# Kernel tuning notes

Measured on AMD Instinct MI355X. Metric: run time of the kernel, lower is better.

## Reference

```python
import jax, jax.numpy as jnp
import numpy as np

N_NODES = 100000
N_EDGES = 1600000
VOCAB = 100000
HIDDEN = 64
OUT = 1
N_REL = 2


def _fast_rgcn_conv(h, src, dst, et, W, root, b, num_nodes, num_rel):
    # Per-relation linear transform of all nodes first (cheap: N*H*O per relation),
    # then gather the transformed source feature for each edge by its relation.
    h_rel = jnp.einsum('nh,rho->rno', h, W)            # (R, N, O)
    msg = h_rel[et, src]                                # (E, O) gather
    # FastRGCNConv 'mean' aggregation: normalize by edge count per (dst, relation)
    one_hot = jax.nn.one_hot(et, num_rel, dtype=h.dtype)            # (E, R)
    counts = jax.ops.segment_sum(one_hot, dst, num_segments=num_nodes)  # (N, R)
    norm = 1.0 / jnp.maximum(counts[dst, et], 1.0)                  # (E,)
    aggr = jax.ops.segment_sum(msg * norm[:, None], dst, num_segments=num_nodes)  # (N, O)
    return aggr + h @ root + b


def setup_inputs() -> dict:
    key = jax.random.key(0)
    k = jax.random.split(key, 8)
    x = jnp.arange(N_NODES, dtype=jnp.int64 if jax.config.read('jax_enable_x64') else jnp.int32)
    edge_index = jax.random.randint(k[0], (2, N_EDGES), 0, N_NODES)
    node_type = jax.random.randint(k[1], (N_NODES,), 0, 2)
    s_h = 1.0 / np.sqrt(HIDDEN)
    emb = jax.random.normal(k[2], (VOCAB, HIDDEN), jnp.float32)
    W1 = jax.random.normal(k[3], (N_REL, HIDDEN, HIDDEN), jnp.float32) * s_h
    root1 = jax.random.normal(k[4], (HIDDEN, HIDDEN), jnp.float32) * s_h
    b1 = jnp.zeros((HIDDEN,), jnp.float32)
    W2 = jax.random.normal(k[5], (N_REL, HIDDEN, OUT), jnp.float32) * s_h
    root2 = jax.random.normal(k[6], (HIDDEN, OUT), jnp.float32) * s_h
    b2 = jnp.zeros((OUT,), jnp.float32)
    return {"x": x, "edge_index": edge_index, "node_type": node_type,
            "emb": emb, "W1": W1, "root1": root1, "b1": b1,
            "W2": W2, "root2": root2, "b2": b2}


def reference(x, edge_index, node_type, emb, W1, root1, b1, W2, root2, b2):
    src, dst = edge_index[0], edge_index[1]
    # edge_type = 1 if same node type else 0
    et = (node_type[src] == node_type[dst]).astype(jnp.int32)
    h = emb[x]                                          # embedding lookup (N, H)
    h = _fast_rgcn_conv(h, src, dst, et, W1, root1, b1, N_NODES, N_REL)
    h = jax.nn.relu(h)
    out = _fast_rgcn_conv(h, src, dst, et, W2, root2, b2, N_NODES, N_REL)
    return out  # (N, 1)
```

## Files before the change

### kernel.cpp

```cpp
#include <hip/hip_runtime.h>

#define N_NODES 100000
#define N_EDGES 1600000
#define HIDDEN 64
#define NBKT 782
#define BKT_SHIFT 7
#define NT 391
#define TILE 4096

typedef __attribute__((ext_vector_type(8))) short short8v;
typedef __attribute__((ext_vector_type(4))) float f32x4;

__device__ __forceinline__ unsigned short f2bf(float f) {
    union { float f; unsigned u; } v; v.f = f;
    return (unsigned short)((v.u + 0x7FFFu + ((v.u >> 16) & 1u)) >> 16);
}
__device__ __forceinline__ float bf2f(unsigned short h) {
    union { unsigned u; float f; } v; v.u = ((unsigned)h) << 16;
    return v.f;
}


__global__ __launch_bounds__(256) void k_embf(const int* __restrict__ x, const float* __restrict__ emb,
                                              unsigned short* __restrict__ embbf) {
    int gid = blockIdx.x * 256 + threadIdx.x;
    int n = gid >> 4, q = gid & 15;
    if (n >= N_NODES) return;
    int row = x[n];
    float4 v = *(const float4*)&emb[(long long)row * HIDDEN + q * 4];
    ushort4 p;
    p.x = f2bf(v.x); p.y = f2bf(v.y); p.z = f2bf(v.z); p.w = f2bf(v.w);
    *(ushort4*)&embbf[n * HIDDEN + q * 4] = p;
}

__global__ __launch_bounds__(512) void k_hist(const int* __restrict__ ei,
                                              const int* __restrict__ ntype,
                                              unsigned* __restrict__ ps,
                                              int* __restrict__ tilecnt) {
    __shared__ int hist[NBKT];
    int tile = blockIdx.x, tid = threadIdx.x;
    for (int i = tid; i < NBKT; i += 512) hist[i] = 0;
    __syncthreads();
    int e0 = tile * TILE;
    int e1 = e0 + TILE; if (e1 > N_EDGES) e1 = N_EDGES;
    for (int e = e0 + tid; e < e1; e += 512) {
        int s = ei[e], d = ei[N_EDGES + e];
        int t = (ntype[s] == ntype[d]) ? 1 : 0;
        ps[e] = ((unsigned)s << 1) | (unsigned)t;
        atomicAdd(&hist[d >> BKT_SHIFT], 1);
    }
    __syncthreads();
    for (int i = tid; i < NBKT; i += 512) tilecnt[tile * NBKT + i] = hist[i];
}

__global__ __launch_bounds__(512) void k_scanA(int* __restrict__ tilecnt, int* __restrict__ btot) {
    __shared__ int sc[512];
    int b = blockIdx.x, tid = threadIdx.x;
    int v = (tid < NT) ? tilecnt[tid * NBKT + b] : 0;
    sc[tid] = v;
    __syncthreads();
    for (int off = 1; off < 512; off <<= 1) {
        int a = sc[tid];
        int p = (tid >= off) ? sc[tid - off] : 0;
        __syncthreads();
        sc[tid] = a + p;
        __syncthreads();
    }
    if (tid < NT) tilecnt[tid * NBKT + b] = sc[tid] - v;
    if (tid == 511) btot[b] = sc[511];
}

__global__ __launch_bounds__(1024) void k_scanB(const int* __restrict__ btot, int* __restrict__ bbase) {
    __shared__ int sc[1024];
    int tid = threadIdx.x;
    int v = (tid < NBKT) ? btot[tid] : 0;
    sc[tid] = v;
    __syncthreads();
    for (int off = 1; off < 1024; off <<= 1) {
        int a = sc[tid];
        int p = (tid >= off) ? sc[tid - off] : 0;
        __syncthreads();
        sc[tid] = a + p;
        __syncthreads();
    }
    if (tid < NBKT) bbase[tid] = sc[tid] - v;
}

__global__ __launch_bounds__(512) void k_place(const int* __restrict__ ei,
                                               const unsigned* __restrict__ ps,
                                               const int* __restrict__ tilecnt,
                                               const int* __restrict__ bbase,
                                               unsigned* __restrict__ tmp) {
    __shared__ int cur[NBKT];
    int tile = blockIdx.x, tid = threadIdx.x;
    for (int i = tid; i < NBKT; i += 512) cur[i] = bbase[i] + tilecnt[tile * NBKT + i];
    __syncthreads();
    int e0 = tile * TILE;
    int e1 = e0 + TILE; if (e1 > N_EDGES) e1 = N_EDGES;
    for (int e = e0 + tid; e < e1; e += 512) {
        int d = ei[N_EDGES + e];
        unsigned entry = ((unsigned)(d & 127) << 18) | ps[e];
        int pos = atomicAdd(&cur[d >> BKT_SHIFT], 1);
        tmp[pos] = entry;
    }
}

__global__ __launch_bounds__(256) void k_sort(const unsigned* __restrict__ tmp,
                                              const int* __restrict__ bbase,
                                              const int* __restrict__ btot,
                                              int* __restrict__ cnt, int* __restrict__ row_ptr,
                                              int* __restrict__ csr) {
    __shared__ int hist[256];
    __shared__ int psum[256];
    int b = blockIdx.x, tid = threadIdx.x;
    hist[tid] = 0;
    __syncthreads();
    int base = bbase[b], m = btot[b];

    for (int i = tid; i < m; i += 256) {
        unsigned pe = tmp[base + i];
        atomicAdd(&hist[(int)((pe >> 17) & 0xFE) | (int)(pe & 1)], 1);
    }
    __syncthreads();

    int h = hist[tid];
    psum[tid] = h;
    __syncthreads();
    for (int off = 1; off < 256; off <<= 1) {
        int a = psum[tid];
        int p = (tid >= off) ? psum[tid - off] : 0;
        __syncthreads();
        psum[tid] = a + p;
        __syncthreads();
    }
    int excl = psum[tid] - h;

    int node = b * 128 + (tid >> 1);
    if (node < N_NODES) {
        cnt[node * 2 + (tid & 1)] = h;
        if ((tid & 1) == 0) row_ptr[node] = base + excl;
    }
    __syncthreads();
    hist[tid] = excl;
    __syncthreads();

    for (int i = tid; i < m; i += 256) {
        unsigned pe = tmp[base + i];
        int bin = (int)((pe >> 17) & 0xFE) | (int)(pe & 1);
        int pos = base + atomicAdd(&hist[bin], 1);
        csr[pos] = (int)((pe >> 1) & 0x1FFFF);
    }
}

__global__ void k_gather1(const int* __restrict__ csr, const int* __restrict__ row_ptr,
                          const int* __restrict__ cnt, const unsigned short* __restrict__ embbf,
                          unsigned short* __restrict__ aggbf) {
    int gid = blockIdx.x * blockDim.x + threadIdx.x;
    int n = gid >> 6;
    int lane = gid & 63;
    if (n >= N_NODES) return;
    int q = lane >> 4;
    int ch = (lane & 15) * 4;
    int beg = row_ptr[n];
    int c0 = cnt[2 * n], c1 = cnt[2 * n + 1];
    int tot = c0 + c1;
    float a00 = 0.f, a01 = 0.f, a02 = 0.f, a03 = 0.f;
    float a10 = 0.f, a11 = 0.f, a12 = 0.f, a13 = 0.f;
    int jj = 0;
    for (; jj + 16 <= tot; jj += 16) {
        int j0 = jj + q, j1 = jj + 4 + q, j2 = jj + 8 + q, j3 = jj + 12 + q;
        int s0 = csr[beg + j0], s1 = csr[beg + j1], s2 = csr[beg + j2], s3 = csr[beg + j3];
        ushort4 v0 = *(const ushort4*)&embbf[s0 * HIDDEN + ch];
        ushort4 v1 = *(const ushort4*)&embbf[s1 * HIDDEN + ch];
        ushort4 v2 = *(const ushort4*)&embbf[s2 * HIDDEN + ch];
        ushort4 v3 = *(const ushort4*)&embbf[s3 * HIDDEN + ch];
        if (j0 < c0) { a00 += bf2f(v0.x); a01 += bf2f(v0.y); a02 += bf2f(v0.z); a03 += bf2f(v0.w); }
        else         { a10 += bf2f(v0.x); a11 += bf2f(v0.y); a12 += bf2f(v0.z); a13 += bf2f(v0.w); }
        if (j1 < c0) { a00 += bf2f(v1.x); a01 += bf2f(v1.y); a02 += bf2f(v1.z); a03 += bf2f(v1.w); }
        else         { a10 += bf2f(v1.x); a11 += bf2f(v1.y); a12 += bf2f(v1.z); a13 += bf2f(v1.w); }
        if (j2 < c0) { a00 += bf2f(v2.x); a01 += bf2f(v2.y); a02 += bf2f(v2.z); a03 += bf2f(v2.w); }
        else         { a10 += bf2f(v2.x); a11 += bf2f(v2.y); a12 += bf2f(v2.z); a13 += bf2f(v2.w); }
        if (j3 < c0) { a00 += bf2f(v3.x); a01 += bf2f(v3.y); a02 += bf2f(v3.z); a03 += bf2f(v3.w); }
        else         { a10 += bf2f(v3.x); a11 += bf2f(v3.y); a12 += bf2f(v3.z); a13 += bf2f(v3.w); }
    }
    for (int j = jj + q; j < tot; j += 4) {
        int s = csr[beg + j];
        ushort4 v = *(const ushort4*)&embbf[s * HIDDEN + ch];
        if (j < c0) { a00 += bf2f(v.x); a01 += bf2f(v.y); a02 += bf2f(v.z); a03 += bf2f(v.w); }
        else        { a10 += bf2f(v.x); a11 += bf2f(v.y); a12 += bf2f(v.z); a13 += bf2f(v.w); }
    }
    a00 += __shfl_xor(a00, 16); a00 += __shfl_xor(a00, 32);
    a01 += __shfl_xor(a01, 16); a01 += __shfl_xor(a01, 32);
    a02 += __shfl_xor(a02, 16); a02 += __shfl_xor(a02, 32);
    a03 += __shfl_xor(a03, 16); a03 += __shfl_xor(a03, 32);
    a10 += __shfl_xor(a10, 16); a10 += __shfl_xor(a10, 32);
    a11 += __shfl_xor(a11, 16); a11 += __shfl_xor(a11, 32);
    a12 += __shfl_xor(a12, 16); a12 += __shfl_xor(a12, 32);
    a13 += __shfl_xor(a13, 16); a13 += __shfl_xor(a13, 32);
    if (q == 0) {
        float n0 = 1.0f / (float)(c0 > 1 ? c0 : 1);
        float n1 = 1.0f / (float)(c1 > 1 ? c1 : 1);
        ushort4 w0, w1;
        w0.x = f2bf(a00 * n0); w0.y = f2bf(a01 * n0); w0.z = f2bf(a02 * n0); w0.w = f2bf(a03 * n0);
        w1.x = f2bf(a10 * n1); w1.y = f2bf(a11 * n1); w1.z = f2bf(a12 * n1); w1.w = f2bf(a13 * n1);
        *(ushort4*)&aggbf[n * 128 + ch] = w0;
        *(ushort4*)&aggbf[n * 128 + 64 + ch] = w1;
    }
}

#define KPAD 200
__global__ __launch_bounds__(256) void k_l1mfma(const unsigned short* __restrict__ embbf,
                                                const unsigned short* __restrict__ aggbf,
                                                const float* __restrict__ W1, const float* __restrict__ root1,
                                                const float* __restrict__ b1,
                                                const float* __restrict__ W2, const float* __restrict__ root2,
                                                const float* __restrict__ b2,
                                                float* __restrict__ s, float* __restrict__ out) {
    __shared__ unsigned short Bw[64][KPAD];
    int tid = threadIdx.x;
    int w = tid >> 6, lane = tid & 63;
    int nodeBase = blockIdx.x * 64;

    for (int it = 0; it < 12; ++it) {
        int f = it * 256 + tid;
        int k = f >> 4, o4 = (f & 15) * 4;
        float4 wv = (k < 128) ? *(const float4*)&W1[k * 64 + o4]
                              : *(const float4*)&root1[(k - 128) * 64 + o4];
        Bw[o4 + 0][k] = f2bf(wv.x);
        Bw[o4 + 1][k] = f2bf(wv.y);
        Bw[o4 + 2][k] = f2bf(wv.z);
        Bw[o4 + 3][k] = f2bf(wv.w);
    }
    __syncthreads();

    int r = lane & 15, g = lane >> 4;
    int node = nodeBase + w * 16 + r;
    int cn = node < N_NODES ? node : 0;
    const unsigned short* arow = &aggbf[cn * 128];
    const unsigned short* erow = &embbf[cn * HIDDEN];
    f32x4 acc0 = {0.f, 0.f, 0.f, 0.f}, acc1 = acc0, acc2 = acc0, acc3 = acc0;
#pragma unroll
    for (int ks = 0; ks < 6; ++ks) {
        int koff = ks * 32 + g * 8;
        short8v av = (ks < 4) ? *(const short8v*)&arow[koff]
                              : *(const short8v*)&erow[koff - 128];
        short8v bv0 = *(const short8v*)&Bw[r][koff];
        short8v bv1 = *(const short8v*)&Bw[16 + r][koff];
        short8v bv2 = *(const short8v*)&Bw[32 + r][koff];
        short8v bv3 = *(const short8v*)&Bw[48 + r][koff];
        acc0 = __builtin_amdgcn_mfma_f32_16x16x32_bf16(av, bv0, acc0, 0, 0, 0);
        acc1 = __builtin_amdgcn_mfma_f32_16x16x32_bf16(av, bv1, acc1, 0, 0, 0);
        acc2 = __builtin_amdgcn_mfma_f32_16x16x32_bf16(av, bv2, acc2, 0, 0, 0);
        acc3 = __builtin_amdgcn_mfma_f32_16x16x32_bf16(av, bv3, acc3, 0, 0, 0);
    }

    float b10 = b1[r], b11 = b1[16 + r], b12 = b1[32 + r], b13 = b1[48 + r];
    float w2a0 = W2[r], w2a1 = W2[16 + r], w2a2 = W2[32 + r], w2a3 = W2[48 + r];
    float w2b0 = W2[64 + r], w2b1 = W2[80 + r], w2b2 = W2[96 + r], w2b3 = W2[112 + r];
    float rr0 = root2[r], rr1 = root2[16 + r], rr2 = root2[32 + r], rr3 = root2[48 + r];
    float b2v = b2[0];
#pragma unroll
    for (int reg = 0; reg < 4; ++reg) {
        float h0 = acc0[reg] + b10; h0 = h0 > 0.f ? h0 : 0.f;
        float h1 = acc1[reg] + b11; h1 = h1 > 0.f ? h1 : 0.f;
        float h2 = acc2[reg] + b12; h2 = h2 > 0.f ? h2 : 0.f;
        float h3 = acc3[reg] + b13; h3 = h3 > 0.f ? h3 : 0.f;
        float p0 = h0 * w2a0 + h1 * w2a1 + h2 * w2a2 + h3 * w2a3;
        float p1 = h0 * w2b0 + h1 * w2b1 + h2 * w2b2 + h3 * w2b3;
        float p2 = h0 * rr0  + h1 * rr1  + h2 * rr2  + h3 * rr3;
#pragma unroll
        for (int mk = 8; mk >= 1; mk >>= 1) {
            p0 += __shfl_xor(p0, mk);
            p1 += __shfl_xor(p1, mk);
            p2 += __shfl_xor(p2, mk);
        }
        if (r == 0) {
            int nd = nodeBase + w * 16 + g * 4 + reg;
            if (nd < N_NODES) {
                s[nd] = p0;
                s[N_NODES + nd] = p1;
                out[nd] = p2 + b2v;
            }
        }
    }
}

__global__ void k_gather2(const int* __restrict__ csr, const int* __restrict__ row_ptr,
                          const int* __restrict__ cnt, const float* __restrict__ sarr,
                          float* __restrict__ out) {
    int gid = blockIdx.x * blockDim.x + threadIdx.x;
    int n = gid >> 4;
    int l = gid & 15;
    if (n >= N_NODES) return;
    int beg = row_ptr[n];
    int c0 = cnt[2 * n], c1 = cnt[2 * n + 1];
    int tot = c0 + c1;
    float n0 = 1.0f / (float)(c0 > 1 ? c0 : 1);
    float n1 = 1.0f / (float)(c1 > 1 ? c1 : 1);
    float acc = 0.f;
    for (int j = l; j < tot; j += 16) {
        int src = csr[beg + j];
        acc += (j < c0) ? sarr[src] * n0 : sarr[N_NODES + src] * n1;
    }
    acc += __shfl_xor(acc, 1);
    acc += __shfl_xor(acc, 2);
    acc += __shfl_xor(acc, 4);
    acc += __shfl_xor(acc, 8);
    if (l == 0) out[n] += acc;
}

extern "C" void kernel_launch(void* const* d_in, const int* in_sizes, int n_in,
                              void* d_out, int out_size, void* d_ws, size_t ws_size,
                              hipStream_t stream) {
    const int* x      = (const int*)d_in[0];
    const int* ei     = (const int*)d_in[1];
    const int* ntype  = (const int*)d_in[2];
    const float* emb  = (const float*)d_in[3];
    const float* W1   = (const float*)d_in[4];
    const float* root1= (const float*)d_in[5];
    const float* b1   = (const float*)d_in[6];
    const float* W2   = (const float*)d_in[7];
    const float* root2= (const float*)d_in[8];
    const float* b2   = (const float*)d_in[9];
    float* out = (float*)d_out;

    char* ws = (char*)d_ws;
    size_t off = 0;
    auto alloc = [&](size_t bytes) -> void* {
        void* p = ws + off;
        off = (off + bytes + 255) & ~(size_t)255;
        return p;
    };
    unsigned* ps           = (unsigned*)alloc((size_t)N_EDGES * sizeof(unsigned));
    int* tilecnt           = (int*)alloc((size_t)NT * NBKT * sizeof(int));
    int* btot              = (int*)alloc((size_t)NBKT * sizeof(int));
    int* bbase             = (int*)alloc((size_t)NBKT * sizeof(int));
    unsigned* tmp          = (unsigned*)alloc((size_t)N_EDGES * sizeof(unsigned));
    int* cnt               = (int*)alloc((size_t)N_NODES * 2 * sizeof(int));
    int* row_ptr           = (int*)alloc((size_t)N_NODES * sizeof(int));
    int* csr               = (int*)alloc((size_t)N_EDGES * sizeof(int));
    unsigned short* embbf  = (unsigned short*)alloc((size_t)N_NODES * HIDDEN * sizeof(unsigned short));
    unsigned short* aggbf  = (unsigned short*)alloc((size_t)N_NODES * 128 * sizeof(unsigned short));
    float* s               = (float*)alloc((size_t)N_NODES * 2 * sizeof(float));

    k_embf <<<(N_NODES * 16 + 255) / 256, 256, 0, stream>>>(x, emb, embbf);
    k_hist <<<NT, 512, 0, stream>>>(ei, ntype, ps, tilecnt);
    k_scanA<<<NBKT, 512, 0, stream>>>(tilecnt, btot);
    k_scanB<<<1, 1024, 0, stream>>>(btot, bbase);
    k_place<<<NT, 512, 0, stream>>>(ei, ps, tilecnt, bbase, tmp);
    k_sort <<<NBKT, 256, 0, stream>>>(tmp, bbase, btot, cnt, row_ptr, csr);
    k_gather1<<<(N_NODES * 64) / 256, 256, 0, stream>>>(csr, row_ptr, cnt, embbf, aggbf);
    k_l1mfma<<<(N_NODES + 63) / 64, 256, 0, stream>>>(embbf, aggbf, W1, root1, b1,
                                                      W2, root2, b2, s, out);
    k_gather2<<<(N_NODES * 16 + 255) / 256, 256, 0, stream>>>(csr, row_ptr, cnt, s, out);
}
```

Before: 149.7 us.

## Fuse layer-1 neighbor gather into MFMA GEMM kernel via shared-memory staging

Merges the per-node mean-aggregation gather into the layer-1 MFMA kernel. Each wavefront gathers its 16 nodes sequentially and writes the bf16 aggregates into an LDS tile, which then feeds the MFMA A operand directly. This removes the global aggbf round trip (write plus reread) and one kernel launch. The cost is less parallelism in the gather: one wave now walks 16 nodes serially instead of one node per wave. LDS use per block also rises, which may reduce occupancy and latency hiding for the random-access gather.

```diff
diff --git a/kernel.cpp b/kernel.cpp
--- a/kernel.cpp
+++ b/kernel.cpp
@@ -152,71 +152,18 @@
     }
 }
 
-__global__ void k_gather1(const int* __restrict__ csr, const int* __restrict__ row_ptr,
-                          const int* __restrict__ cnt, const unsigned short* __restrict__ embbf,
-                          unsigned short* __restrict__ aggbf) {
-    int gid = blockIdx.x * blockDim.x + threadIdx.x;
-    int n = gid >> 6;
-    int lane = gid & 63;
-    if (n >= N_NODES) return;
-    int q = lane >> 4;
-    int ch = (lane & 15) * 4;
-    int beg = row_ptr[n];
-    int c0 = cnt[2 * n], c1 = cnt[2 * n + 1];
-    int tot = c0 + c1;
-    float a00 = 0.f, a01 = 0.f, a02 = 0.f, a03 = 0.f;
-    float a10 = 0.f, a11 = 0.f, a12 = 0.f, a13 = 0.f;
-    int jj = 0;
-    for (; jj + 16 <= tot; jj += 16) {
-        int j0 = jj + q, j1 = jj + 4 + q, j2 = jj + 8 + q, j3 = jj + 12 + q;
-        int s0 = csr[beg + j0], s1 = csr[beg + j1], s2 = csr[beg + j2], s3 = csr[beg + j3];
-        ushort4 v0 = *(const ushort4*)&embbf[s0 * HIDDEN + ch];
-        ushort4 v1 = *(const ushort4*)&embbf[s1 * HIDDEN + ch];
-        ushort4 v2 = *(const ushort4*)&embbf[s2 * HIDDEN + ch];
-        ushort4 v3 = *(const ushort4*)&embbf[s3 * HIDDEN + ch];
-        if (j0 < c0) { a00 += bf2f(v0.x); a01 += bf2f(v0.y); a02 += bf2f(v0.z); a03 += bf2f(v0.w); }
-        else         { a10 += bf2f(v0.x); a11 += bf2f(v0.y); a12 += bf2f(v0.z); a13 += bf2f(v0.w); }
-        if (j1 < c0) { a00 += bf2f(v1.x); a01 += bf2f(v1.y); a02 += bf2f(v1.z); a03 += bf2f(v1.w); }
-        else         { a10 += bf2f(v1.x); a11 += bf2f(v1.y); a12 += bf2f(v1.z); a13 += bf2f(v1.w); }
-        if (j2 < c0) { a00 += bf2f(v2.x); a01 += bf2f(v2.y); a02 += bf2f(v2.z); a03 += bf2f(v2.w); }
-        else         { a10 += bf2f(v2.x); a11 += bf2f(v2.y); a12 += bf2f(v2.z); a13 += bf2f(v2.w); }
-        if (j3 < c0) { a00 += bf2f(v3.x); a01 += bf2f(v3.y); a02 += bf2f(v3.z); a03 += bf2f(v3.w); }
-        else         { a10 += bf2f(v3.x); a11 += bf2f(v3.y); a12 += bf2f(v3.z); a13 += bf2f(v3.w); }
-    }
-    for (int j = jj + q; j < tot; j += 4) {
-        int s = csr[beg + j];
-        ushort4 v = *(const ushort4*)&embbf[s * HIDDEN + ch];
-        if (j < c0) { a00 += bf2f(v.x); a01 += bf2f(v.y); a02 += bf2f(v.z); a03 += bf2f(v.w); }
-        else        { a10 += bf2f(v.x); a11 += bf2f(v.y); a12 += bf2f(v.z); a13 += bf2f(v.w); }
-    }
-    a00 += __shfl_xor(a00, 16); a00 += __shfl_xor(a00, 32);
-    a01 += __shfl_xor(a01, 16); a01 += __shfl_xor(a01, 32);
-    a02 += __shfl_xor(a02, 16); a02 += __shfl_xor(a02, 32);
-    a03 += __shfl_xor(a03, 16); a03 += __shfl_xor(a03, 32);
-    a10 += __shfl_xor(a10, 16); a10 += __shfl_xor(a10, 32);
-    a11 += __shfl_xor(a11, 16); a11 += __shfl_xor(a11, 32);
-    a12 += __shfl_xor(a12, 16); a12 += __shfl_xor(a12, 32);
-    a13 += __shfl_xor(a13, 16); a13 += __shfl_xor(a13, 32);
-    if (q == 0) {
-        float n0 = 1.0f / (float)(c0 > 1 ? c0 : 1);
-        float n1 = 1.0f / (float)(c1 > 1 ? c1 : 1);
-        ushort4 w0, w1;
-        w0.x = f2bf(a00 * n0); w0.y = f2bf(a01 * n0); w0.z = f2bf(a02 * n0); w0.w = f2bf(a03 * n0);
-        w1.x = f2bf(a10 * n1); w1.y = f2bf(a11 * n1); w1.z = f2bf(a12 * n1); w1.w = f2bf(a13 * n1);
-        *(ushort4*)&aggbf[n * 128 + ch] = w0;
-        *(ushort4*)&aggbf[n * 128 + 64 + ch] = w1;
-    }
-}
-
-#define KPAD 200
-__global__ __launch_bounds__(256) void k_l1mfma(const unsigned short* __restrict__ embbf,
-                                                const unsigned short* __restrict__ aggbf,
-                                                const float* __restrict__ W1, const float* __restrict__ root1,
-                                                const float* __restrict__ b1,
-                                                const float* __restrict__ W2, const float* __restrict__ root2,
-                                                const float* __restrict__ b2,
-                                                float* __restrict__ s, float* __restrict__ out) {
-    __shared__ unsigned short Bw[64][KPAD];
+#define KPADA 136
+#define KPADB 200
+__global__ __launch_bounds__(256) void k_fused(const int* __restrict__ csr, const int* __restrict__ row_ptr,
+                                               const int* __restrict__ cnt,
+                                               const unsigned short* __restrict__ embbf,
+                                               const float* __restrict__ W1, const float* __restrict__ root1,
+                                               const float* __restrict__ b1,
+                                               const float* __restrict__ W2, const float* __restrict__ root2,
+                                               const float* __restrict__ b2,
+                                               float* __restrict__ s, float* __restrict__ out) {
+    __shared__ unsigned short Aw[4][16][KPADA];
+    __shared__ unsigned short Bw[64][KPADB];
     int tid = threadIdx.x;
     int w = tid >> 6, lane = tid & 63;
     int nodeBase = blockIdx.x * 64;
@@ -231,18 +178,69 @@
         Bw[o4 + 2][k] = f2bf(wv.z);
         Bw[o4 + 3][k] = f2bf(wv.w);
     }
+
+    int q = lane >> 4;
+    int ch = (lane & 15) * 4;
+    for (int nd = 0; nd < 16; ++nd) {
+        int n = nodeBase + w * 16 + nd;
+        if (n >= N_NODES) break;
+        int beg = row_ptr[n];
+        int c0 = cnt[2 * n], c1 = cnt[2 * n + 1];
+        int tot = c0 + c1;
+        float a00 = 0.f, a01 = 0.f, a02 = 0.f, a03 = 0.f;
+        float a10 = 0.f, a11 = 0.f, a12 = 0.f, a13 = 0.f;
+        int jj = 0;
+        for (; jj + 16 <= tot; jj += 16) {
+            int j0 = jj + q, j1 = jj + 4 + q, j2 = jj + 8 + q, j3 = jj + 12 + q;
+            int s0 = csr[beg + j0], s1 = csr[beg + j1], s2 = csr[beg + j2], s3 = csr[beg + j3];
+            ushort4 v0 = *(const ushort4*)&embbf[s0 * HIDDEN + ch];
+            ushort4 v1 = *(const ushort4*)&embbf[s1 * HIDDEN + ch];
+            ushort4 v2 = *(const ushort4*)&embbf[s2 * HIDDEN + ch];
+            ushort4 v3 = *(const ushort4*)&embbf[s3 * HIDDEN + ch];
+            if (j0 < c0) { a00 += bf2f(v0.x); a01 += bf2f(v0.y); a02 += bf2f(v0.z); a03 += bf2f(v0.w); }
+            else         { a10 += bf2f(v0.x); a11 += bf2f(v0.y); a12 += bf2f(v0.z); a13 += bf2f(v0.w); }
+            if (j1 < c0) { a00 += bf2f(v1.x); a01 += bf2f(v1.y); a02 += bf2f(v1.z); a03 += bf2f(v1.w); }
+            else         { a10 += bf2f(v1.x); a11 += bf2f(v1.y); a12 += bf2f(v1.z); a13 += bf2f(v1.w); }
+            if (j2 < c0) { a00 += bf2f(v2.x); a01 += bf2f(v2.y); a02 += bf2f(v2.z); a03 += bf2f(v2.w); }
+            else         { a10 += bf2f(v2.x); a11 += bf2f(v2.y); a12 += bf2f(v2.z); a13 += bf2f(v2.w); }
+            if (j3 < c0) { a00 += bf2f(v3.x); a01 += bf2f(v3.y); a02 += bf2f(v3.z); a03 += bf2f(v3.w); }
+            else         { a10 += bf2f(v3.x); a11 += bf2f(v3.y); a12 += bf2f(v3.z); a13 += bf2f(v3.w); }
+        }
+        for (int j = jj + q; j < tot; j += 4) {
+            int sv = csr[beg + j];
+            ushort4 v = *(const ushort4*)&embbf[sv * HIDDEN + ch];
+            if (j < c0) { a00 += bf2f(v.x); a01 += bf2f(v.y); a02 += bf2f(v.z); a03 += bf2f(v.w); }
+            else        { a10 += bf2f(v.x); a11 += bf2f(v.y); a12 += bf2f(v.z); a13 += bf2f(v.w); }
+        }
+        a00 += __shfl_xor(a00, 16); a00 += __shfl_xor(a00, 32);
+        a01 += __shfl_xor(a01, 16); a01 += __shfl_xor(a01, 32);
+        a02 += __shfl_xor(a02, 16); a02 += __shfl_xor(a02, 32);
+        a03 += __shfl_xor(a03, 16); a03 += __shfl_xor(a03, 32);
+        a10 += __shfl_xor(a10, 16); a10 += __shfl_xor(a10, 32);
+        a11 += __shfl_xor(a11, 16); a11 += __shfl_xor(a11, 32);
+        a12 += __shfl_xor(a12, 16); a12 += __shfl_xor(a12, 32);
+        a13 += __shfl_xor(a13, 16); a13 += __shfl_xor(a13, 32);
+        if (q == 0) {
+            float n0 = 1.0f / (float)(c0 > 1 ? c0 : 1);
+            float n1 = 1.0f / (float)(c1 > 1 ? c1 : 1);
+            ushort4 w0, w1;
+            w0.x = f2bf(a00 * n0); w0.y = f2bf(a01 * n0); w0.z = f2bf(a02 * n0); w0.w = f2bf(a03 * n0);
+            w1.x = f2bf(a10 * n1); w1.y = f2bf(a11 * n1); w1.z = f2bf(a12 * n1); w1.w = f2bf(a13 * n1);
+            *(ushort4*)&Aw[w][nd][ch] = w0;
+            *(ushort4*)&Aw[w][nd][64 + ch] = w1;
+        }
+    }
     __syncthreads();
 
     int r = lane & 15, g = lane >> 4;
     int node = nodeBase + w * 16 + r;
     int cn = node < N_NODES ? node : 0;
-    const unsigned short* arow = &aggbf[cn * 128];
     const unsigned short* erow = &embbf[cn * HIDDEN];
     f32x4 acc0 = {0.f, 0.f, 0.f, 0.f}, acc1 = acc0, acc2 = acc0, acc3 = acc0;
 #pragma unroll
     for (int ks = 0; ks < 6; ++ks) {
         int koff = ks * 32 + g * 8;
-        short8v av = (ks < 4) ? *(const short8v*)&arow[koff]
+        short8v av = (ks < 4) ? *(const short8v*)&Aw[w][r][koff]
                               : *(const short8v*)&erow[koff - 128];
         short8v bv0 = *(const short8v*)&Bw[r][koff];
         short8v bv1 = *(const short8v*)&Bw[16 + r][koff];
@@ -340,7 +338,6 @@
     int* row_ptr           = (int*)alloc((size_t)N_NODES * sizeof(int));
     int* csr               = (int*)alloc((size_t)N_EDGES * sizeof(int));
     unsigned short* embbf  = (unsigned short*)alloc((size_t)N_NODES * HIDDEN * sizeof(unsigned short));
-    unsigned short* aggbf  = (unsigned short*)alloc((size_t)N_NODES * 128 * sizeof(unsigned short));
     float* s               = (float*)alloc((size_t)N_NODES * 2 * sizeof(float));
 
     k_embf <<<(N_NODES * 16 + 255) / 256, 256, 0, stream>>>(x, emb, embbf);
@@ -349,8 +346,7 @@
     k_scanB<<<1, 1024, 0, stream>>>(btot, bbase);
     k_place<<<NT, 512, 0, stream>>>(ei, ps, tilecnt, bbase, tmp);
     k_sort <<<NBKT, 256, 0, stream>>>(tmp, bbase, btot, cnt, row_ptr, csr);
-    k_gather1<<<(N_NODES * 64) / 256, 256, 0, stream>>>(csr, row_ptr, cnt, embbf, aggbf);
-    k_l1mfma<<<(N_NODES + 63) / 64, 256, 0, stream>>>(embbf, aggbf, W1, root1, b1,
-                                                      W2, root2, b2, s, out);
+    k_fused<<<(N_NODES + 63) / 64, 256, 0, stream>>>(csr, row_ptr, cnt, embbf,
+                                                     W1, root1, b1, W2, root2, b2, s, out);
     k_gather2<<<(N_NODES * 16 + 255) / 256, 256, 0, stream>>>(csr, row_ptr, cnt, s, out);
 }
```

Measured after the change: 209.8 us. 1.4x slower.

## Fuse embedding cast, histogram and weight prep into one pre-kernel; precount degrees

Applied to the files above, without the earlier changes.

Merges the embedding bf16 conversion and edge histogram kernels into one launch with block-range dispatch, and adds a block that converts W1/root1 to a transposed bf16 matrix once. Per-(node,relation) counts are now built with global atomics during the histogram pass, so k_sort drops its counting pass over the bucket. The MFMA layer-1 kernel reads B fragments straight from global instead of converting weights into LDS in every block. The trade-off is 1.6M global atomics on cnt, an extra memset, and uncached global B reads in place of LDS.

```diff
diff --git a/kernel.cpp b/kernel.cpp
--- a/kernel.cpp
+++ b/kernel.cpp
@@ -7,6 +7,7 @@
 #define BKT_SHIFT 7
 #define NT 391
 #define TILE 4096
+#define EMBF_BLKS 3125
 
 typedef __attribute__((ext_vector_type(8))) short short8v;
 typedef __attribute__((ext_vector_type(4))) float f32x4;
@@ -21,36 +22,50 @@
 }
 
 
-__global__ __launch_bounds__(256) void k_embf(const int* __restrict__ x, const float* __restrict__ emb,
-                                              unsigned short* __restrict__ embbf) {
-    int gid = blockIdx.x * 256 + threadIdx.x;
-    int n = gid >> 4, q = gid & 15;
-    if (n >= N_NODES) return;
-    int row = x[n];
-    float4 v = *(const float4*)&emb[(long long)row * HIDDEN + q * 4];
-    ushort4 p;
-    p.x = f2bf(v.x); p.y = f2bf(v.y); p.z = f2bf(v.z); p.w = f2bf(v.w);
-    *(ushort4*)&embbf[n * HIDDEN + q * 4] = p;
-}
-
-__global__ __launch_bounds__(512) void k_hist(const int* __restrict__ ei,
-                                              const int* __restrict__ ntype,
-                                              unsigned* __restrict__ ps,
-                                              int* __restrict__ tilecnt) {
+__global__ __launch_bounds__(512) void k_pre(const int* __restrict__ ei,
+                                             const int* __restrict__ ntype,
+                                             const int* __restrict__ x,
+                                             const float* __restrict__ emb,
+                                             const float* __restrict__ W1,
+                                             const float* __restrict__ root1,
+                                             unsigned* __restrict__ ps,
+                                             int* __restrict__ tilecnt,
+                                             int* __restrict__ cnt,
+                                             unsigned short* __restrict__ embbf,
+                                             unsigned short* __restrict__ Bbf) {
     __shared__ int hist[NBKT];
-    int tile = blockIdx.x, tid = threadIdx.x;
-    for (int i = tid; i < NBKT; i += 512) hist[i] = 0;
-    __syncthreads();
-    int e0 = tile * TILE;
-    int e1 = e0 + TILE; if (e1 > N_EDGES) e1 = N_EDGES;
-    for (int e = e0 + tid; e < e1; e += 512) {
-        int s = ei[e], d = ei[N_EDGES + e];
-        int t = (ntype[s] == ntype[d]) ? 1 : 0;
-        ps[e] = ((unsigned)s << 1) | (unsigned)t;
-        atomicAdd(&hist[d >> BKT_SHIFT], 1);
-    }
-    __syncthreads();
-    for (int i = tid; i < NBKT; i += 512) tilecnt[tile * NBKT + i] = hist[i];
+    int bid = blockIdx.x, tid = threadIdx.x;
+    if (bid < NT) {
+        for (int i = tid; i < NBKT; i += 512) hist[i] = 0;
+        __syncthreads();
+        int e0 = bid * TILE;
+        int e1 = e0 + TILE; if (e1 > N_EDGES) e1 = N_EDGES;
+        for (int e = e0 + tid; e < e1; e += 512) {
+            int s = ei[e], d = ei[N_EDGES + e];
+            int t = (ntype[s] == ntype[d]) ? 1 : 0;
+            ps[e] = ((unsigned)s << 1) | (unsigned)t;
+            atomicAdd(&hist[d >> BKT_SHIFT], 1);
+            atomicAdd(&cnt[d * 2 + t], 1);
+        }
+        __syncthreads();
+        for (int i = tid; i < NBKT; i += 512) tilecnt[bid * NBKT + i] = hist[i];
+    } else if (bid < NT + EMBF_BLKS) {
+        int gid = (bid - NT) * 512 + tid;
+        int n = gid >> 4, q = gid & 15;
+        if (n < N_NODES) {
+            int row = x[n];
+            float4 v = *(const float4*)&emb[(long long)row * HIDDEN + q * 4];
+            ushort4 p;
+            p.x = f2bf(v.x); p.y = f2bf(v.y); p.z = f2bf(v.z); p.w = f2bf(v.w);
+            *(ushort4*)&embbf[n * HIDDEN + q * 4] = p;
+        }
+    } else {
+        for (int e = tid; e < 192 * 64; e += 512) {
+            int o = e / 192, k = e - o * 192;
+            float v = (k < 128) ? W1[k * 64 + o] : root1[(k - 128) * 64 + o];
+            Bbf[e] = f2bf(v);
+        }
+    }
 }
 
 __global__ __launch_bounds__(512) void k_scanA(int* __restrict__ tilecnt, int* __restrict__ btot) {
@@ -108,22 +123,16 @@
 __global__ __launch_bounds__(256) void k_sort(const unsigned* __restrict__ tmp,
                                               const int* __restrict__ bbase,
                                               const int* __restrict__ btot,
-                                              int* __restrict__ cnt, int* __restrict__ row_ptr,
+                                              const int* __restrict__ cnt,
+                                              int* __restrict__ row_ptr,
                                               int* __restrict__ csr) {
-    __shared__ int hist[256];
+    __shared__ int cur[256];
     __shared__ int psum[256];
     int b = blockIdx.x, tid = threadIdx.x;
-    hist[tid] = 0;
-    __syncthreads();
     int base = bbase[b], m = btot[b];
-
-    for (int i = tid; i < m; i += 256) {
-        unsigned pe = tmp[base + i];
-        atomicAdd(&hist[(int)((pe >> 17) & 0xFE) | (int)(pe & 1)], 1);
-    }
-    __syncthreads();
-
-    int h = hist[tid];
+    int node = b * 128 + (tid >> 1);
+    int h = (node < N_NODES) ? cnt[b * 256 + tid] : 0;
+
     psum[tid] = h;
     __syncthreads();
     for (int off = 1; off < 256; off <<= 1) {
@@ -134,20 +143,14 @@
         __syncthreads();
     }
     int excl = psum[tid] - h;
-
-    int node = b * 128 + (tid >> 1);
-    if (node < N_NODES) {
-        cnt[node * 2 + (tid & 1)] = h;
-        if ((tid & 1) == 0) row_ptr[node] = base + excl;
-    }
-    __syncthreads();
-    hist[tid] = excl;
+    if (node < N_NODES && (tid & 1) == 0) row_ptr[node] = base + excl;
+    cur[tid] = excl;
     __syncthreads();
 
     for (int i = tid; i < m; i += 256) {
         unsigned pe = tmp[base + i];
         int bin = (int)((pe >> 17) & 0xFE) | (int)(pe & 1);
-        int pos = base + atomicAdd(&hist[bin], 1);
+        int pos = base + atomicAdd(&cur[bin], 1);
         csr[pos] = (int)((pe >> 1) & 0x1FFFF);
     }
 }
@@ -208,30 +211,16 @@
     }
 }
 
-#define KPAD 200
 __global__ __launch_bounds__(256) void k_l1mfma(const unsigned short* __restrict__ embbf,
                                                 const unsigned short* __restrict__ aggbf,
-                                                const float* __restrict__ W1, const float* __restrict__ root1,
+                                                const unsigned short* __restrict__ Bbf,
                                                 const float* __restrict__ b1,
                                                 const float* __restrict__ W2, const float* __restrict__ root2,
                                                 const float* __restrict__ b2,
                                                 float* __restrict__ s, float* __restrict__ out) {
-    __shared__ unsigned short Bw[64][KPAD];
     int tid = threadIdx.x;
     int w = tid >> 6, lane = tid & 63;
     int nodeBase = blockIdx.x * 64;
-
-    for (int it = 0; it < 12; ++it) {
-        int f = it * 256 + tid;
-        int k = f >> 4, o4 = (f & 15) * 4;
-        float4 wv = (k < 128) ? *(const float4*)&W1[k * 64 + o4]
-                              : *(const float4*)&root1[(k - 128) * 64 + o4];
-        Bw[o4 + 0][k] = f2bf(wv.x);
-        Bw[o4 + 1][k] = f2bf(wv.y);
-        Bw[o4 + 2][k] = f2bf(wv.z);
-        Bw[o4 + 3][k] = f2bf(wv.w);
-    }
-    __syncthreads();
 
     int r = lane & 15, g = lane >> 4;
     int node = nodeBase + w * 16 + r;
@@ -244,10 +233,10 @@
         int koff = ks * 32 + g * 8;
         short8v av = (ks < 4) ? *(const short8v*)&arow[koff]
                               : *(const short8v*)&erow[koff - 128];
-        short8v bv0 = *(const short8v*)&Bw[r][koff];
-        short8v bv1 = *(const short8v*)&Bw[16 + r][koff];
-        short8v bv2 = *(const short8v*)&Bw[32 + r][koff];
-        short8v bv3 = *(const short8v*)&Bw[48 + r][koff];
+        short8v bv0 = *(const short8v*)&Bbf[r * 192 + koff];
+        short8v bv1 = *(const short8v*)&Bbf[(16 + r) * 192 + koff];
+        short8v bv2 = *(const short8v*)&Bbf[(32 + r) * 192 + koff];
+        short8v bv3 = *(const short8v*)&Bbf[(48 + r) * 192 + koff];
         acc0 = __builtin_amdgcn_mfma_f32_16x16x32_bf16(av, bv0, acc0, 0, 0, 0);
         acc1 = __builtin_amdgcn_mfma_f32_16x16x32_bf16(av, bv1, acc1, 0, 0, 0);
         acc2 = __builtin_amdgcn_mfma_f32_16x16x32_bf16(av, bv2, acc2, 0, 0, 0);
@@ -341,16 +330,19 @@
     int* csr               = (int*)alloc((size_t)N_EDGES * sizeof(int));
     unsigned short* embbf  = (unsigned short*)alloc((size_t)N_NODES * HIDDEN * sizeof(unsigned short));
     unsigned short* aggbf  = (unsigned short*)alloc((size_t)N_NODES * 128 * sizeof(unsigned short));
+    unsigned short* Bbf    = (unsigned short*)alloc((size_t)192 * 64 * sizeof(unsigned short));
     float* s               = (float*)alloc((size_t)N_NODES * 2 * sizeof(float));
 
-    k_embf <<<(N_NODES * 16 + 255) / 256, 256, 0, stream>>>(x, emb, embbf);
-    k_hist <<<NT, 512, 0, stream>>>(ei, ntype, ps, tilecnt);
+    hipMemsetAsync(cnt, 0, (size_t)N_NODES * 2 * sizeof(int), stream);
+
+    k_pre  <<<NT + EMBF_BLKS + 1, 512, 0, stream>>>(ei, ntype, x, emb, W1, root1,
+                                                    ps, tilecnt, cnt, embbf, Bbf);
     k_scanA<<<NBKT, 512, 0, stream>>>(tilecnt, btot);
     k_scanB<<<1, 1024, 0, stream>>>(btot, bbase);
     k_place<<<NT, 512, 0, stream>>>(ei, ps, tilecnt, bbase, tmp);
     k_sort <<<NBKT, 256, 0, stream>>>(tmp, bbase, btot, cnt, row_ptr, csr);
     k_gather1<<<(N_NODES * 64) / 256, 256, 0, stream>>>(csr, row_ptr, cnt, embbf, aggbf);
-    k_l1mfma<<<(N_NODES + 63) / 64, 256, 0, stream>>>(embbf, aggbf, W1, root1, b1,
+    k_l1mfma<<<(N_NODES + 63) / 64, 256, 0, stream>>>(embbf, aggbf, Bbf, b1,
                                                       W2, root2, b2, s, out);
     k_gather2<<<(N_NODES * 16 + 255) / 256, 256, 0, stream>>>(csr, row_ptr, cnt, s, out);
 }
```

Result: slower. 206.0 us (+37.6%).
